# Performance work log

Measured on AMD Instinct MI355X. Metric: run time of the kernel, lower is better.

The kernel has to match this reference:

```python
import jax, jax.numpy as jnp
import numpy as np

B, S, V, H, K, T = 4, 256, 32000, 1024, 4, 20
THRESHOLD = 0.6


def setup_inputs() -> dict:
    key = jax.random.key(0)
    ks = jax.random.split(key, 12)
    sH = 1.0 / np.sqrt(H)
    return {
        "input_ids": jax.random.randint(ks[0], (B, S), 0, V),
        "labels": jax.random.randint(ks[1], (B, S), 0, V),
        "embed": jax.random.normal(ks[2], (V, H), jnp.float32) * 0.02,
        "W1": jax.random.normal(ks[3], (H, H), jnp.float32) * sH,
        "b1": jnp.zeros((H,), jnp.float32),
        "lm_head": jax.random.normal(ks[4], (H, V), jnp.float32) * 0.02,
        "W_gen": jax.random.normal(ks[5], (H, H), jnp.float32) * sH,
        "thought_emb": jax.random.normal(ks[6], (K, H), jnp.float32) * 0.02,
        "tpos_emb": jax.random.normal(ks[7], (T, H), jnp.float32) * 0.02,
        "w_score": jax.random.normal(ks[8], (2 * H,), jnp.float32) * sH,
        "w_gate": jax.random.normal(ks[9], (2 * H,), jnp.float32) * sH,
    }


def reference(input_ids, labels, embed, W1, b1, lm_head, W_gen,
              thought_emb, tpos_emb, w_score, w_gate):
    # ---- base model: embed -> tanh MLP -> lm_head ----
    h0 = embed[input_ids]                                 # (B,S,H)
    hidden = jnp.tanh(h0 @ W1 + b1)                       # base last_hidden_state
    base_logits = hidden @ lm_head                        # (B,S,V)

    # ---- ThoughtInjector: per-position gate from normalized entropy ----
    logp = jax.nn.log_softmax(base_logits, axis=-1)
    ent = -jnp.sum(jnp.exp(logp) * logp, axis=-1) / jnp.log(float(V))  # (B,S)
    inject = (ent.mean(axis=0) > THRESHOLD) & (jnp.arange(S) < S - 1)   # (S,)

    # ---- ThoughtGenerator: (B,S,K,T,H) thoughts (masked dispatch, all pos) ----
    g = jnp.tanh(hidden @ W_gen)                          # (B,S,H)
    thoughts = jnp.tanh(g[:, :, None, None, :]
                        + thought_emb[None, None, :, None, :]
                        + tpos_emb[None, None, None, :, :])  # (B,S,K,T,H)
    tmean = thoughts.mean(axis=3)                         # (B,S,K,H) = thoughts.mean(dim=2)

    # ---- CoherenceScorer: composite score per thought ----
    comp = jax.nn.sigmoid(
        jnp.einsum('bsh,h->bs', hidden, w_score[:H])[:, :, None]
        + jnp.einsum('bskh,h->bsk', tmean, w_score[H:]))  # (B,S,K)

    # ---- MixingHead: coherence-weighted thought mix, gated blend with hidden ----
    alpha = jax.nn.softmax(comp, axis=-1)                 # (B,S,K)
    mixed_thought = jnp.einsum('bsk,bskh->bsh', alpha, tmean)
    gate = jax.nn.sigmoid(jnp.einsum('bsh,h->bs', hidden, w_gate[:H])
                          + jnp.einsum('bsh,h->bs', mixed_thought, w_gate[H:]))[..., None]
    mixed = gate * mixed_thought + (1.0 - gate) * hidden

    enhanced = jnp.where(inject[None, :, None], mixed, hidden)
    final_logits = enhanced @ lm_head                     # (B,S,V)

    # ---- shifted cross-entropy loss ----
    sl = jax.nn.log_softmax(final_logits[:, :-1, :], axis=-1)
    loss = -jnp.take_along_axis(sl, labels[:, 1:, None], axis=-1).mean()
    return final_logits, loss
```

## Files before the change

### kernel.cpp

```cpp
#include <hip/hip_runtime.h>


#define V_SZ 32000
#define H_SZ 1024
#define S_SZ 256
#define B_SZ 4
#define M_SZ 1024
#define K_TH 4
#define T_TH 20

typedef __bf16 bf16_t;
typedef __bf16 bf16x8 __attribute__((ext_vector_type(8)));
typedef __bf16 bf16x4 __attribute__((ext_vector_type(4)));
typedef float  f32x4  __attribute__((ext_vector_type(4)));

__device__ __forceinline__ float tanh_fast(float x) {
  x = fminf(fmaxf(x, -15.f), 15.f);
  float e = __expf(2.f * x);
  return (e - 1.f) / (e + 1.f);
}
__device__ __forceinline__ float sigmoid_f(float x) {
  return 1.f / (1.f + __expf(-x));
}

__global__ void __launch_bounds__(256) transpose_cast_kernel(
    const float* __restrict__ in, bf16_t* __restrict__ out, int R, int C) {
  __shared__ float tile[32][33];
  const int tx = threadIdx.x & 31, ty = threadIdx.x >> 5;
  const int c0 = blockIdx.x << 5, r0 = blockIdx.y << 5;
  #pragma unroll
  for (int i = ty; i < 32; i += 8)
    tile[i][tx] = in[(size_t)(r0 + i) * C + c0 + tx];
  __syncthreads();
  #pragma unroll
  for (int i = ty; i < 32; i += 8)
    out[(size_t)(c0 + i) * R + r0 + tx] = (bf16_t)tile[tx][i];
}

__global__ void __launch_bounds__(256) gather_cast_kernel(
    const int* __restrict__ ids, const float* __restrict__ embed,
    bf16_t* __restrict__ X0) {
  const int i = blockIdx.x * 256 + threadIdx.x;
  const int m = i >> 8, c4 = (i & 255) << 2;
  const float4 v = *(const float4*)(embed + (size_t)ids[m] * H_SZ + c4);
  bf16x4 o;
  o[0] = (bf16_t)v.x; o[1] = (bf16_t)v.y; o[2] = (bf16_t)v.z; o[3] = (bf16_t)v.w;
  *(bf16x4*)(X0 + (size_t)m * H_SZ + c4) = o;
}

template <int EPI>
__global__ void __launch_bounds__(256, 2) gemm_bt(
    const bf16_t* __restrict__ A, const bf16_t* __restrict__ BT,
    float* __restrict__ outF, bf16_t* __restrict__ outB,
    const float* __restrict__ bias, int mtiles, int ntiles, int N) {
  __shared__ __align__(16) bf16_t As[128 * 40];
  __shared__ __align__(16) bf16_t Bs[128 * 40];
  const int t = threadIdx.x;
  const int x = blockIdx.x & 7, y = blockIdx.x >> 3;
  const int tm = y % mtiles, tn = x + 8 * (y / mtiles);
  if (tn >= ntiles) return;
  const int m0 = tm * 128, n0 = tn * 128;
  const int lane = t & 63, wv = t >> 6, wm = wv >> 1, wn = wv & 1;
  const int col = lane & 15, qd = lane >> 4;
  const int ldr = t >> 2, ldk = (t & 3) * 8;
  f32x4 acc[4][4] = {};
  for (int kb = 0; kb < 1024; kb += 32) {
    #pragma unroll
    for (int c = 0; c < 2; ++c) {
      const int row = ldr + 64 * c;
      uint4 av = *(const uint4*)(A  + (size_t)(m0 + row) * 1024 + kb + ldk);
      uint4 bv = *(const uint4*)(BT + (size_t)(n0 + row) * 1024 + kb + ldk);
      *(uint4*)(As + row * 40 + ldk) = av;
      *(uint4*)(Bs + row * 40 + ldk) = bv;
    }
    __syncthreads();
    bf16x8 af[4], bg[4];
    #pragma unroll
    for (int mi = 0; mi < 4; ++mi)
      af[mi] = *(const bf16x8*)(As + (wm * 64 + mi * 16 + col) * 40 + qd * 8);
    #pragma unroll
    for (int ni = 0; ni < 4; ++ni)
      bg[ni] = *(const bf16x8*)(Bs + (wn * 64 + ni * 16 + col) * 40 + qd * 8);
    #pragma unroll
    for (int mi = 0; mi < 4; ++mi)
      #pragma unroll
      for (int ni = 0; ni < 4; ++ni)
        acc[mi][ni] = __builtin_amdgcn_mfma_f32_16x16x32_bf16(
            af[mi], bg[ni], acc[mi][ni], 0, 0, 0);
    __syncthreads();
  }
  #pragma unroll
  for (int mi = 0; mi < 4; ++mi) {
    #pragma unroll
    for (int ni = 0; ni < 4; ++ni) {
      const int gm = m0 + wm * 64 + mi * 16 + qd * 4;
      const int gn = n0 + wn * 64 + ni * 16 + col;
      #pragma unroll
      for (int r = 0; r < 4; ++r) {
        const size_t o = (size_t)(gm + r) * N + gn;
        float v = acc[mi][ni][r];
        if (EPI == 1) {
          v = tanh_fast(v + bias[gn]);
          outF[o] = v;
          outB[o] = (bf16_t)v;
        } else if (EPI == 2) {
          outF[o] = tanh_fast(v);
        } else {
          outF[o] = v;
        }
      }
    }
  }
}

__global__ void __launch_bounds__(256) entropy_kernel(
    const float* __restrict__ logits, float* __restrict__ ent) {
  const int row = blockIdx.x, t = threadIdx.x;
  const float* l = logits + (size_t)row * V_SZ;
  float m = l[t], Z = 1.f, Sv = 0.f;
  for (int i = t + 256; i < V_SZ; i += 256) {
    const float xv = l[i];
    if (xv > m) {
      const float c = __expf(m - xv);
      Sv = c * (Sv + (m - xv) * Z);
      Z = c * Z + 1.f;
      m = xv;
    } else {
      const float e = __expf(xv - m);
      Z += e;
      Sv += e * (xv - m);
    }
  }
  __shared__ float sm[256], sz[256], ss[256];
  sm[t] = m; sz[t] = Z; ss[t] = Sv;
  __syncthreads();
  for (int off = 128; off > 0; off >>= 1) {
    if (t < off) {
      const float m1 = sm[t], z1 = sz[t], s1 = ss[t];
      const float m2 = sm[t + off], z2 = sz[t + off], s2 = ss[t + off];
      const float mm = fmaxf(m1, m2);
      const float c1 = __expf(m1 - mm), c2 = __expf(m2 - mm);
      sm[t] = mm;
      sz[t] = z1 * c1 + z2 * c2;
      ss[t] = (s1 + (m1 - mm) * z1) * c1 + (s2 + (m2 - mm) * z2) * c2;
    }
    __syncthreads();
  }
  if (t == 0) ent[row] = __logf(sz[0]) - ss[0] / sz[0];
}

__global__ void __launch_bounds__(256) inject_kernel(
    const float* __restrict__ ent, int* __restrict__ inject) {
  const int s = threadIdx.x;
  const float e = 0.25f * (ent[s] + ent[S_SZ + s] + ent[2 * S_SZ + s] + ent[3 * S_SZ + s]);
  inject[s] = (e * (1.0f / 10.373491f) > 0.6f) && (s < S_SZ - 1) ? 1 : 0;
}

__global__ void __launch_bounds__(256) thoughts_kernel(
    const float* __restrict__ g, const float* __restrict__ th_emb,
    const float* __restrict__ tpos, float* __restrict__ tmean) {
  const int idx = blockIdx.x * 256 + threadIdx.x;
  const int h = idx & (H_SZ - 1);
  const int mk = idx >> 10;
  const int kk = mk & (K_TH - 1);
  const int m = mk >> 2;
  const float base = g[(size_t)m * H_SZ + h] + th_emb[kk * H_SZ + h];
  float s = 0.f;
  #pragma unroll
  for (int tt = 0; tt < T_TH; ++tt) s += tanh_fast(base + tpos[tt * H_SZ + h]);
  tmean[idx] = s * (1.f / T_TH);
}

__device__ __forceinline__ float block_sum(float v, float* red, int t) {
  red[t] = v;
  __syncthreads();
  for (int off = 128; off > 0; off >>= 1) {
    if (t < off) red[t] += red[t + off];
    __syncthreads();
  }
  const float r = red[0];
  __syncthreads();
  return r;
}

__global__ void __launch_bounds__(256) mix_kernel(
    const float* __restrict__ hidden, const float* __restrict__ tmean,
    const float* __restrict__ w_score, const float* __restrict__ w_gate,
    const int* __restrict__ inject, bf16_t* __restrict__ enhB) {
  const int m = blockIdx.x, t = threadIdx.x, s = m & (S_SZ - 1);
  __shared__ float red[256];
  float hv[4], ws1[4], ws2[4], wg1[4], wg2[4], tmv[4][4];
  #pragma unroll
  for (int j = 0; j < 4; ++j) {
    const int h = t + 256 * j;
    hv[j]  = hidden[(size_t)m * H_SZ + h];
    ws1[j] = w_score[h];      ws2[j] = w_score[H_SZ + h];
    wg1[j] = w_gate[h];       wg2[j] = w_gate[H_SZ + h];
    #pragma unroll
    for (int k = 0; k < 4; ++k) tmv[k][j] = tmean[(size_t)(m * 4 + k) * H_SZ + h];
  }
  float ph = 0.f, pg = 0.f;
  #pragma unroll
  for (int j = 0; j < 4; ++j) { ph += hv[j] * ws1[j]; pg += hv[j] * wg1[j]; }
  const float sh = block_sum(ph, red, t);
  const float gh = block_sum(pg, red, t);
  float comp[4];
  #pragma unroll
  for (int k = 0; k < 4; ++k) {
    float pc = 0.f;
    #pragma unroll
    for (int j = 0; j < 4; ++j) pc += tmv[k][j] * ws2[j];
    const float ck = block_sum(pc, red, t);
    comp[k] = sigmoid_f(sh + ck);
  }
  const float ma = fmaxf(fmaxf(comp[0], comp[1]), fmaxf(comp[2], comp[3]));
  float al[4], asum = 0.f;
  #pragma unroll
  for (int k = 0; k < 4; ++k) { al[k] = __expf(comp[k] - ma); asum += al[k]; }
  const float inv = 1.f / asum;
  float mx[4];
  #pragma unroll
  for (int j = 0; j < 4; ++j) {
    mx[j] = 0.f;
    #pragma unroll
    for (int k = 0; k < 4; ++k) mx[j] += al[k] * inv * tmv[k][j];
  }
  float pm = 0.f;
  #pragma unroll
  for (int j = 0; j < 4; ++j) pm += mx[j] * wg2[j];
  const float gm = block_sum(pm, red, t);
  const float gate = sigmoid_f(gh + gm);
  const int inj = inject[s];
  #pragma unroll
  for (int j = 0; j < 4; ++j) {
    const float e = inj ? (gate * mx[j] + (1.f - gate) * hv[j]) : hv[j];
    enhB[(size_t)m * H_SZ + t + 256 * j] = (bf16_t)e;
  }
}

__global__ void __launch_bounds__(256) lse_kernel(
    const float* __restrict__ logits, float* __restrict__ lse) {
  const int row = blockIdx.x, t = threadIdx.x;
  const float* l = logits + (size_t)row * V_SZ;
  float m = l[t], Z = 1.f;
  for (int i = t + 256; i < V_SZ; i += 256) {
    const float xv = l[i];
    if (xv > m) { Z = Z * __expf(m - xv) + 1.f; m = xv; }
    else        { Z += __expf(xv - m); }
  }
  __shared__ float sm[256], sz[256];
  sm[t] = m; sz[t] = Z;
  __syncthreads();
  for (int off = 128; off > 0; off >>= 1) {
    if (t < off) {
      const float m1 = sm[t], z1 = sz[t], m2 = sm[t + off], z2 = sz[t + off];
      const float mm = fmaxf(m1, m2);
      sz[t] = z1 * __expf(m1 - mm) + z2 * __expf(m2 - mm);
      sm[t] = mm;
    }
    __syncthreads();
  }
  if (t == 0) lse[row] = sm[0] + __logf(sz[0]);
}

__global__ void __launch_bounds__(256) loss_kernel(
    const float* __restrict__ logits, const float* __restrict__ lse,
    const int* __restrict__ labels, float* __restrict__ out_loss) {
  const int t = threadIdx.x;
  float acc = 0.f;
  for (int i = t; i < (S_SZ - 1) * B_SZ; i += 256) {
    const int b = i / (S_SZ - 1), s2 = i % (S_SZ - 1);
    const int m = b * S_SZ + s2;
    const int lab = labels[m + 1];
    acc += lse[m] - logits[(size_t)m * V_SZ + lab];
  }
  __shared__ float red[256];
  red[t] = acc;
  __syncthreads();
  for (int off = 128; off > 0; off >>= 1) {
    if (t < off) red[t] += red[t + off];
    __syncthreads();
  }
  if (t == 0) out_loss[0] = red[0] / (float)((S_SZ - 1) * B_SZ);
}

extern "C" void kernel_launch(void* const* d_in, const int* in_sizes, int n_in,
                              void* d_out, int out_size, void* d_ws, size_t ws_size,
                              hipStream_t stream) {
  const int*   ids    = (const int*)  d_in[0];
  const int*   labels = (const int*)  d_in[1];
  const float* embed  = (const float*)d_in[2];
  const float* W1     = (const float*)d_in[3];
  const float* b1     = (const float*)d_in[4];
  const float* lm     = (const float*)d_in[5];
  const float* Wg     = (const float*)d_in[6];
  const float* thE    = (const float*)d_in[7];
  const float* tpos   = (const float*)d_in[8];
  const float* wsc    = (const float*)d_in[9];
  const float* wgt    = (const float*)d_in[10];
  float* out = (float*)d_out;

  char* p = (char*)d_ws;
  auto carve = [&p](size_t bytes) {
    char* r = p;
    p += (bytes + 255) & ~(size_t)255;
    return r;
  };
  bf16_t* lmT   = (bf16_t*)carve((size_t)V_SZ * H_SZ * sizeof(bf16_t));
  bf16_t* W1T   = (bf16_t*)carve((size_t)H_SZ * H_SZ * sizeof(bf16_t));
  bf16_t* WgT   = (bf16_t*)carve((size_t)H_SZ * H_SZ * sizeof(bf16_t));
  bf16_t* X0    = (bf16_t*)carve((size_t)M_SZ * H_SZ * sizeof(bf16_t));
  bf16_t* hidB  = (bf16_t*)carve((size_t)M_SZ * H_SZ * sizeof(bf16_t));
  bf16_t* enhB  = (bf16_t*)carve((size_t)M_SZ * H_SZ * sizeof(bf16_t));
  float*  hidF  = (float*) carve((size_t)M_SZ * H_SZ * sizeof(float));
  float*  gF    = (float*) carve((size_t)M_SZ * H_SZ * sizeof(float));
  float*  tmean = (float*) carve((size_t)M_SZ * K_TH * H_SZ * sizeof(float));
  float*  ent   = (float*) carve(M_SZ * sizeof(float));
  float*  lse   = (float*) carve(M_SZ * sizeof(float));
  int*    inj   = (int*)   carve(S_SZ * sizeof(int));

  transpose_cast_kernel<<<dim3(V_SZ / 32, H_SZ / 32), 256, 0, stream>>>(lm, lmT, H_SZ, V_SZ);
  transpose_cast_kernel<<<dim3(H_SZ / 32, H_SZ / 32), 256, 0, stream>>>(W1, W1T, H_SZ, H_SZ);
  transpose_cast_kernel<<<dim3(H_SZ / 32, H_SZ / 32), 256, 0, stream>>>(Wg, WgT, H_SZ, H_SZ);
  gather_cast_kernel<<<M_SZ * H_SZ / 4 / 256, 256, 0, stream>>>(ids, embed, X0);

  gemm_bt<1><<<64, 256, 0, stream>>>(X0, W1T, hidF, hidB, b1, 8, 8, H_SZ);
  gemm_bt<2><<<64, 256, 0, stream>>>(hidB, WgT, gF, nullptr, nullptr, 8, 8, H_SZ);
  gemm_bt<0><<<2048, 256, 0, stream>>>(hidB, lmT, out, nullptr, nullptr, 8, 250, V_SZ);

  entropy_kernel<<<M_SZ, 256, 0, stream>>>(out, ent);
  inject_kernel<<<1, 256, 0, stream>>>(ent, inj);
  thoughts_kernel<<<M_SZ * K_TH * H_SZ / 256, 256, 0, stream>>>(gF, thE, tpos, tmean);
  mix_kernel<<<M_SZ, 256, 0, stream>>>(hidF, tmean, wsc, wgt, inj, enhB);

  gemm_bt<0><<<2048, 256, 0, stream>>>(enhB, lmT, out, nullptr, nullptr, 8, 250, V_SZ);
  lse_kernel<<<M_SZ, 256, 0, stream>>>(out, lse);
  loss_kernel<<<1, 256, 0, stream>>>(out, lse, labels, out + (size_t)M_SZ * V_SZ);
}
```

Baseline: 680.8 us.

## Fuse entropy and logsumexp reductions into lm_head GEMM epilogues

```diff
diff --git a/kernel.cpp b/kernel.cpp
--- a/kernel.cpp
+++ b/kernel.cpp
@@ -8,6 +8,8 @@
 #define M_SZ 1024
 #define K_TH 4
 #define T_TH 20
+#define NTILE_V 250
+#define PARTS (NTILE_V * 2)
 
 typedef __bf16 bf16_t;
 typedef __bf16 bf16x8 __attribute__((ext_vector_type(8)));
@@ -52,9 +54,10 @@
 __global__ void __launch_bounds__(256, 2) gemm_bt(
     const bf16_t* __restrict__ A, const bf16_t* __restrict__ BT,
     float* __restrict__ outF, bf16_t* __restrict__ outB,
-    const float* __restrict__ bias, int mtiles, int ntiles, int N) {
-  __shared__ __align__(16) bf16_t As[128 * 40];
-  __shared__ __align__(16) bf16_t Bs[128 * 40];
+    const float* __restrict__ bias, float2* __restrict__ entP,
+    float* __restrict__ lseP, int mtiles, int ntiles, int N) {
+  __shared__ __align__(16) bf16_t As[128 * 32];
+  __shared__ __align__(16) bf16_t Bs[128 * 32];
   const int t = threadIdx.x;
   const int x = blockIdx.x & 7, y = blockIdx.x >> 3;
   const int tm = y % mtiles, tn = x + 8 * (y / mtiles);
@@ -62,25 +65,35 @@
   const int m0 = tm * 128, n0 = tn * 128;
   const int lane = t & 63, wv = t >> 6, wm = wv >> 1, wn = wv & 1;
   const int col = lane & 15, qd = lane >> 4;
-  const int ldr = t >> 2, ldk = (t & 3) * 8;
+  const int ldr = t >> 2, ldch = t & 3;
+  const int st0 = ldr * 32 + ((ldch ^ ((ldr >> 1) & 3)) << 3);
+  const int st1 = (ldr + 64) * 32 + ((ldch ^ ((ldr >> 1) & 3)) << 3);
+  int offA[4], offB[4];
+  #pragma unroll
+  for (int i = 0; i < 4; ++i) {
+    const int ra = wm * 64 + i * 16 + col;
+    offA[i] = ra * 32 + ((qd ^ ((ra >> 1) & 3)) << 3);
+    const int rb = wn * 64 + i * 16 + col;
+    offB[i] = rb * 32 + ((qd ^ ((rb >> 1) & 3)) << 3);
+  }
   f32x4 acc[4][4] = {};
   for (int kb = 0; kb < 1024; kb += 32) {
-    #pragma unroll
-    for (int c = 0; c < 2; ++c) {
-      const int row = ldr + 64 * c;
-      uint4 av = *(const uint4*)(A  + (size_t)(m0 + row) * 1024 + kb + ldk);
-      uint4 bv = *(const uint4*)(BT + (size_t)(n0 + row) * 1024 + kb + ldk);
-      *(uint4*)(As + row * 40 + ldk) = av;
-      *(uint4*)(Bs + row * 40 + ldk) = bv;
+    {
+      uint4 a0 = *(const uint4*)(A  + (size_t)(m0 + ldr) * 1024 + kb + ldch * 8);
+      uint4 b0 = *(const uint4*)(BT + (size_t)(n0 + ldr) * 1024 + kb + ldch * 8);
+      uint4 a1 = *(const uint4*)(A  + (size_t)(m0 + ldr + 64) * 1024 + kb + ldch * 8);
+      uint4 b1 = *(const uint4*)(BT + (size_t)(n0 + ldr + 64) * 1024 + kb + ldch * 8);
+      *(uint4*)(As + st0) = a0;
+      *(uint4*)(Bs + st0) = b0;
+      *(uint4*)(As + st1) = a1;
+      *(uint4*)(Bs + st1) = b1;
     }
     __syncthreads();
     bf16x8 af[4], bg[4];
     #pragma unroll
-    for (int mi = 0; mi < 4; ++mi)
-      af[mi] = *(const bf16x8*)(As + (wm * 64 + mi * 16 + col) * 40 + qd * 8);
-    #pragma unroll
-    for (int ni = 0; ni < 4; ++ni)
-      bg[ni] = *(const bf16x8*)(Bs + (wn * 64 + ni * 16 + col) * 40 + qd * 8);
+    for (int mi = 0; mi < 4; ++mi) af[mi] = *(const bf16x8*)(As + offA[mi]);
+    #pragma unroll
+    for (int ni = 0; ni < 4; ++ni) bg[ni] = *(const bf16x8*)(Bs + offB[ni]);
     #pragma unroll
     for (int mi = 0; mi < 4; ++mi)
       #pragma unroll
@@ -89,6 +102,51 @@
             af[mi], bg[ni], acc[mi][ni], 0, 0, 0);
     __syncthreads();
   }
+
+  if (EPI == 3 || EPI == 4) {
+    float z[16], s[16];
+    #pragma unroll
+    for (int mi = 0; mi < 4; ++mi) {
+      #pragma unroll
+      for (int rr = 0; rr < 4; ++rr) {
+        float zz = 0.f, ss = 0.f;
+        #pragma unroll
+        for (int ni = 0; ni < 4; ++ni) {
+          const float xv = acc[mi][ni][rr];
+          const float e = __expf(xv);
+          zz += e;
+          if (EPI == 3) ss += xv * e;
+          if (EPI == 4) {
+            const size_t o = (size_t)(m0 + wm * 64 + mi * 16 + qd * 4 + rr) * N
+                           + (n0 + wn * 64 + ni * 16 + col);
+            outF[o] = xv;
+          }
+        }
+        z[mi * 4 + rr] = zz;
+        s[mi * 4 + rr] = ss;
+      }
+    }
+    #pragma unroll
+    for (int d = 1; d < 16; d <<= 1) {
+      #pragma unroll
+      for (int i = 0; i < 16; ++i) {
+        z[i] += __shfl_xor(z[i], d);
+        if (EPI == 3) s[i] += __shfl_xor(s[i], d);
+      }
+    }
+    if (col == 0) {
+      #pragma unroll
+      for (int i = 0; i < 16; ++i) {
+        const int row = m0 + wm * 64 + (i >> 2) * 16 + qd * 4 + (i & 3);
+        if (EPI == 3)
+          entP[(size_t)row * PARTS + tn * 2 + wn] = make_float2(z[i], s[i]);
+        else
+          lseP[(size_t)row * PARTS + tn * 2 + wn] = z[i];
+      }
+    }
+    return;
+  }
+
   #pragma unroll
   for (int mi = 0; mi < 4; ++mi) {
     #pragma unroll
@@ -113,47 +171,39 @@
   }
 }
 
-__global__ void __launch_bounds__(256) entropy_kernel(
-    const float* __restrict__ logits, float* __restrict__ ent) {
-  const int row = blockIdx.x, t = threadIdx.x;
-  const float* l = logits + (size_t)row * V_SZ;
-  float m = l[t], Z = 1.f, Sv = 0.f;
-  for (int i = t + 256; i < V_SZ; i += 256) {
-    const float xv = l[i];
-    if (xv > m) {
-      const float c = __expf(m - xv);
-      Sv = c * (Sv + (m - xv) * Z);
-      Z = c * Z + 1.f;
-      m = xv;
-    } else {
-      const float e = __expf(xv - m);
-      Z += e;
-      Sv += e * (xv - m);
-    }
-  }
-  __shared__ float sm[256], sz[256], ss[256];
-  sm[t] = m; sz[t] = Z; ss[t] = Sv;
-  __syncthreads();
-  for (int off = 128; off > 0; off >>= 1) {
-    if (t < off) {
-      const float m1 = sm[t], z1 = sz[t], s1 = ss[t];
-      const float m2 = sm[t + off], z2 = sz[t + off], s2 = ss[t + off];
-      const float mm = fmaxf(m1, m2);
-      const float c1 = __expf(m1 - mm), c2 = __expf(m2 - mm);
-      sm[t] = mm;
-      sz[t] = z1 * c1 + z2 * c2;
-      ss[t] = (s1 + (m1 - mm) * z1) * c1 + (s2 + (m2 - mm) * z2) * c2;
-    }
-    __syncthreads();
-  }
-  if (t == 0) ent[row] = __logf(sz[0]) - ss[0] / sz[0];
-}
-
-__global__ void __launch_bounds__(256) inject_kernel(
-    const float* __restrict__ ent, int* __restrict__ inject) {
-  const int s = threadIdx.x;
-  const float e = 0.25f * (ent[s] + ent[S_SZ + s] + ent[2 * S_SZ + s] + ent[3 * S_SZ + s]);
-  inject[s] = (e * (1.0f / 10.373491f) > 0.6f) && (s < S_SZ - 1) ? 1 : 0;
+__global__ void __launch_bounds__(256) ent_inject_kernel(
+    const float2* __restrict__ entP, int* __restrict__ inject) {
+  const int s = blockIdx.x, t = threadIdx.x;
+  const int b = t >> 6, lane = t & 63;
+  const int row = b * S_SZ + s;
+  float z = 0.f, sv = 0.f;
+  for (int i = lane; i < PARTS; i += 64) {
+    const float2 p = entP[(size_t)row * PARTS + i];
+    z += p.x; sv += p.y;
+  }
+  #pragma unroll
+  for (int d = 1; d < 64; d <<= 1) {
+    z += __shfl_xor(z, d);
+    sv += __shfl_xor(sv, d);
+  }
+  __shared__ float se[4];
+  if (lane == 0) se[b] = __logf(z) - sv / z;
+  __syncthreads();
+  if (t == 0) {
+    const float e = 0.25f * (se[0] + se[1] + se[2] + se[3]);
+    inject[s] = (e * (1.0f / 10.373491f) > 0.6f) && (s < S_SZ - 1) ? 1 : 0;
+  }
+}
+
+__global__ void __launch_bounds__(256) lse_merge_kernel(
+    const float* __restrict__ lseP, float* __restrict__ lse) {
+  const int t = threadIdx.x, w = t >> 6, lane = t & 63;
+  const int row = blockIdx.x * 4 + w;
+  float z = 0.f;
+  for (int i = lane; i < PARTS; i += 64) z += lseP[(size_t)row * PARTS + i];
+  #pragma unroll
+  for (int d = 1; d < 64; d <<= 1) z += __shfl_xor(z, d);
+  if (lane == 0) lse[row] = __logf(z);
 }
 
 __global__ void __launch_bounds__(256) thoughts_kernel(
@@ -236,31 +286,6 @@
     const float e = inj ? (gate * mx[j] + (1.f - gate) * hv[j]) : hv[j];
     enhB[(size_t)m * H_SZ + t + 256 * j] = (bf16_t)e;
   }
-}
-
-__global__ void __launch_bounds__(256) lse_kernel(
-    const float* __restrict__ logits, float* __restrict__ lse) {
-  const int row = blockIdx.x, t = threadIdx.x;
-  const float* l = logits + (size_t)row * V_SZ;
-  float m = l[t], Z = 1.f;
-  for (int i = t + 256; i < V_SZ; i += 256) {
-    const float xv = l[i];
-    if (xv > m) { Z = Z * __expf(m - xv) + 1.f; m = xv; }
-    else        { Z += __expf(xv - m); }
-  }
-  __shared__ float sm[256], sz[256];
-  sm[t] = m; sz[t] = Z;
-  __syncthreads();
-  for (int off = 128; off > 0; off >>= 1) {
-    if (t < off) {
-      const float m1 = sm[t], z1 = sz[t], m2 = sm[t + off], z2 = sz[t + off];
-      const float mm = fmaxf(m1, m2);
-      sz[t] = z1 * __expf(m1 - mm) + z2 * __expf(m2 - mm);
-      sm[t] = mm;
-    }
-    __syncthreads();
-  }
-  if (t == 0) lse[row] = sm[0] + __logf(sz[0]);
 }
 
 __global__ void __launch_bounds__(256) loss_kernel(
@@ -315,25 +340,25 @@
   float*  hidF  = (float*) carve((size_t)M_SZ * H_SZ * sizeof(float));
   float*  gF    = (float*) carve((size_t)M_SZ * H_SZ * sizeof(float));
   float*  tmean = (float*) carve((size_t)M_SZ * K_TH * H_SZ * sizeof(float));
-  float*  ent   = (float*) carve(M_SZ * sizeof(float));
   float*  lse   = (float*) carve(M_SZ * sizeof(float));
   int*    inj   = (int*)   carve(S_SZ * sizeof(int));
+  float2* entP = (float2*)tmean;
+  float*  lseP = (float*)tmean;
 
   transpose_cast_kernel<<<dim3(V_SZ / 32, H_SZ / 32), 256, 0, stream>>>(lm, lmT, H_SZ, V_SZ);
   transpose_cast_kernel<<<dim3(H_SZ / 32, H_SZ / 32), 256, 0, stream>>>(W1, W1T, H_SZ, H_SZ);
   transpose_cast_kernel<<<dim3(H_SZ / 32, H_SZ / 32), 256, 0, stream>>>(Wg, WgT, H_SZ, H_SZ);
   gather_cast_kernel<<<M_SZ * H_SZ / 4 / 256, 256, 0, stream>>>(ids, embed, X0);
 
-  gemm_bt<1><<<64, 256, 0, stream>>>(X0, W1T, hidF, hidB, b1, 8, 8, H_SZ);
-  gemm_bt<2><<<64, 256, 0, stream>>>(hidB, WgT, gF, nullptr, nullptr, 8, 8, H_SZ);
-  gemm_bt<0><<<2048, 256, 0, stream>>>(hidB, lmT, out, nullptr, nullptr, 8, 250, V_SZ);
-
-  entropy_kernel<<<M_SZ, 256, 0, stream>>>(out, ent);
-  inject_kernel<<<1, 256, 0, stream>>>(ent, inj);
+  gemm_bt<1><<<64, 256, 0, stream>>>(X0, W1T, hidF, hidB, b1, nullptr, nullptr, 8, 8, H_SZ);
+  gemm_bt<2><<<64, 256, 0, stream>>>(hidB, WgT, gF, nullptr, nullptr, nullptr, nullptr, 8, 8, H_SZ);
+  gemm_bt<3><<<2048, 256, 0, stream>>>(hidB, lmT, nullptr, nullptr, nullptr, entP, nullptr, 8, NTILE_V, V_SZ);
+  ent_inject_kernel<<<S_SZ, 256, 0, stream>>>(entP, inj);
+
   thoughts_kernel<<<M_SZ * K_TH * H_SZ / 256, 256, 0, stream>>>(gF, thE, tpos, tmean);
   mix_kernel<<<M_SZ, 256, 0, stream>>>(hidF, tmean, wsc, wgt, inj, enhB);
 
-  gemm_bt<0><<<2048, 256, 0, stream>>>(enhB, lmT, out, nullptr, nullptr, 8, 250, V_SZ);
-  lse_kernel<<<M_SZ, 256, 0, stream>>>(out, lse);
+  gemm_bt<4><<<2048, 256, 0, stream>>>(enhB, lmT, out, nullptr, nullptr, nullptr, lseP, 8, NTILE_V, V_SZ);
+  lse_merge_kernel<<<M_SZ / 4, 256, 0, stream>>>(lseP, lse);
   loss_kernel<<<1, 256, 0, stream>>>(out, lse, labels, out + (size_t)M_SZ * V_SZ);
 }
```

Result: faster. 602.0 us (-11.6%).
